# Kernel tuning notes

Measured on AMD Instinct MI355X. Metric: run time of the kernel, lower is better.

Reference implementation:

```python
import jax, jax.numpy as jnp
import numpy as np

B, T, D, H = 4, 1024, 1024, 16
DH = D // H  # 64

def setup_inputs() -> dict:
    key = jax.random.key(0)
    ks = jax.random.split(key, 5)
    s = 1.0 / np.sqrt(D)
    return {
        "x": jax.random.normal(ks[0], (B, T, D), dtype=jnp.float32),
        "Wqkv": jax.random.uniform(ks[1], (D, 3 * D), dtype=jnp.float32, minval=-s, maxval=s),
        "bqkv": jax.random.uniform(ks[2], (3 * D,), dtype=jnp.float32, minval=-s, maxval=s),
        "Wproj": jax.random.uniform(ks[3], (D, D), dtype=jnp.float32, minval=-s, maxval=s),
        "bproj": jax.random.uniform(ks[4], (D,), dtype=jnp.float32, minval=-s, maxval=s),
        "mask": jnp.ones((B, T), dtype=jnp.int32),
    }

def reference(x, Wqkv, bqkv, Wproj, bproj, mask):
    Bx, Tx, C = x.shape
    qkv = x @ Wqkv + bqkv                      # [B,T,3D]
    q, k, v = jnp.split(qkv, 3, axis=-1)
    # [B,H,T,DH]
    q = q.reshape(Bx, Tx, H, DH).transpose(0, 2, 1, 3)
    k = k.reshape(Bx, Tx, H, DH).transpose(0, 2, 1, 3)
    v = v.reshape(Bx, Tx, H, DH).transpose(0, 2, 1, 3)
    att = jnp.einsum("bhqd,bhkd->bhqk", q, k) / np.sqrt(DH)
    causal = jnp.tril(jnp.ones((Tx, Tx), dtype=bool))          # [T,T]
    keep = causal[None, None] & (mask[:, None, None, :] != 0)  # [B,1,T,T] broadcast
    att = jnp.where(keep, att, -jnp.inf)
    att = jax.nn.softmax(att, axis=-1)
    # dropout is identity in eval / p=0
    out = jnp.einsum("bhqk,bhkd->bhqd", att, v)                # [B,H,T,DH]
    out = out.transpose(0, 2, 1, 3).reshape(Bx, Tx, C)
    return out @ Wproj + bproj
```

## Files before the change

### kernel.cpp

```cpp
#include <hip/hip_runtime.h>
#include <hip/hip_bf16.h>
#include <cstddef>
#include <cstdint>

#define Bb 4
#define Tt 1024
#define Dd 1024
#define Hh 16

typedef __bf16 bf16x8 __attribute__((ext_vector_type(8)));
typedef __bf16 bf16x4 __attribute__((ext_vector_type(4)));
typedef float  f32x4  __attribute__((ext_vector_type(4)));

__device__ __forceinline__ void gload16(const void* g, void* l) {
    __builtin_amdgcn_global_load_lds(
        (const __attribute__((address_space(1))) void*)g,
        (__attribute__((address_space(3))) void*)l, 16, 0, 0);
}

__global__ __launch_bounds__(256) void prep(const float* __restrict__ x,
                                            const float* __restrict__ Wqkv,
                                            const float* __restrict__ Wproj,
                                            __bf16* __restrict__ xb,
                                            __bf16* __restrict__ wqT,
                                            __bf16* __restrict__ wpT) {
    const int bid = blockIdx.x;
    if (bid < 4096) {
        int i = bid * 256 + threadIdx.x;
        float4 v = ((const float4*)x)[i];
        bf16x4 o = { (__bf16)v.x, (__bf16)v.y, (__bf16)v.z, (__bf16)v.w };
        ((bf16x4*)xb)[i] = o;
        return;
    }
    __shared__ float ld[64][65];
    const float* in;
    __bf16* out;
    int K, N, k0, n0;
    if (bid < 4096 + 768) {
        int j = bid - 4096;
        in = Wqkv; out = wqT; K = 1024; N = 3072;
        k0 = (j & 15) * 64; n0 = (j >> 4) * 64;
    } else {
        int j = bid - 4096 - 768;
        in = Wproj; out = wpT; K = 1024; N = 1024;
        k0 = (j & 15) * 64; n0 = (j >> 4) * 64;
    }
    #pragma unroll
    for (int i = 0; i < 16; i++) {
        int idx = i * 256 + threadIdx.x;
        int r = idx >> 6, c = idx & 63;
        ld[r][c] = in[(size_t)(k0 + r) * N + n0 + c];
    }
    __syncthreads();
    #pragma unroll
    for (int i = 0; i < 16; i++) {
        int idx = i * 256 + threadIdx.x;
        int r = idx >> 6, c = idx & 63;
        out[(size_t)(n0 + r) * K + k0 + c] = (__bf16)ld[c][r];
    }
}

__global__ __launch_bounds__(256) void gemm_qkv(const __bf16* __restrict__ A,
                                                const __bf16* __restrict__ Bt,
                                                const float* __restrict__ bias,
                                                __bf16* __restrict__ Cout,
                                                __bf16* __restrict__ vt,
                                                int M, int N, int K) {
    __shared__ __align__(16) __bf16 smem[17408];
    __bf16* const As = smem;
    __bf16* const Bs = smem + 8192;

    const int tid  = threadIdx.x;
    const int lane = tid & 63;
    const int wave = tid >> 6;
    const int wy = wave >> 1, wx = wave & 1;
    const int l15 = lane & 15, quad = lane >> 4;
    const size_t row0 = (size_t)blockIdx.y * 128;
    const size_t col0 = (size_t)blockIdx.x * 128;

    f32x4 acc[4][4] = {};

    #pragma unroll
    for (int i = 0; i < 2; i++) {
        int c = i * 256 + tid;
        int r = c >> 2, seg = (c & 3) ^ ((r >> 1) & 3);
        gload16(&A[(row0 + r) * K + seg * 8], &As[c * 8]);
        gload16(&Bt[(col0 + r) * K + seg * 8], &Bs[c * 8]);
    }

    const int niter = K >> 5;
    for (int it = 0; it < niter; it++) {
        __syncthreads();
        const int cur = it & 1;
        if (it + 1 < niter) {
            const int k0 = (it + 1) << 5;
            #pragma unroll
            for (int i = 0; i < 2; i++) {
                int c = i * 256 + tid;
                int r = c >> 2, seg = (c & 3) ^ ((r >> 1) & 3);
                gload16(&A[(row0 + r) * K + k0 + seg * 8], &As[(cur ^ 1) * 4096 + c * 8]);
                gload16(&Bt[(col0 + r) * K + k0 + seg * 8], &Bs[(cur ^ 1) * 4096 + c * 8]);
            }
        }
        bf16x8 af[4], bfr[4];
        #pragma unroll
        for (int i = 0; i < 4; i++) {
            const int r = wy * 64 + i * 16 + l15;
            af[i] = *(const bf16x8*)&As[cur * 4096 + r * 32 + ((quad ^ ((r >> 1) & 3)) * 8)];
        }
        #pragma unroll
        for (int j = 0; j < 4; j++) {
            const int r = wx * 64 + j * 16 + l15;
            bfr[j] = *(const bf16x8*)&Bs[cur * 4096 + r * 32 + ((quad ^ ((r >> 1) & 3)) * 8)];
        }
        #pragma unroll
        for (int i = 0; i < 4; i++)
            #pragma unroll
            for (int j = 0; j < 4; j++)
                acc[i][j] = __builtin_amdgcn_mfma_f32_16x16x32_bf16(af[i], bfr[j], acc[i][j], 0, 0, 0);
    }

    __syncthreads();
    #pragma unroll
    for (int j = 0; j < 4; j++) {
        const int cl = wx * 64 + j * 16 + l15;
        const size_t col = col0 + cl;
        const float bj = bias[col];
        const float scale = (col < 1024) ? 0.125f : 1.0f;
        #pragma unroll
        for (int i = 0; i < 4; i++) {
            const int rl = wy * 64 + i * 16 + quad * 4;
            #pragma unroll
            for (int r = 0; r < 4; r++)
                smem[(rl + r) * 132 + cl] = (__bf16)((acc[i][j][r] + bj) * scale);
        }
    }
    __syncthreads();
    #pragma unroll
    for (int p = 0; p < 8; p++) {
        const int row = p * 16 + (tid >> 4);
        const int ch  = tid & 15;
        bf16x8 v = *(const bf16x8*)&smem[row * 132 + ch * 8];
        *(bf16x8*)&Cout[(row0 + row) * N + col0 + ch * 8] = v;
    }
    if (col0 >= 2048) {
        const int bidx = (int)(row0 >> 10);
        const int t0g  = (int)(row0 & 1023);
        const int cl   = tid >> 1;
        const int half = tid & 1;
        const int hd   = (int)(col0 - 2048) + cl;
        const size_t vrow = ((size_t)((bidx * Hh + (hd >> 6)) * 64 + (hd & 63))) * Tt + t0g;
        #pragma unroll
        for (int s = 0; s < 8; s++) {
            const int t = half * 64 + s * 8;
            bf16x8 v;
            #pragma unroll
            for (int u = 0; u < 8; u++) v[u] = smem[(t + u) * 132 + cl];
            *(bf16x8*)&vt[vrow + t] = v;
        }
    }
}

__global__ __launch_bounds__(256) void gemm_bf16_n64(const __bf16* __restrict__ A,
                                                     const __bf16* __restrict__ Bt,
                                                     const float* __restrict__ bias,
                                                     float* __restrict__ Cout,
                                                     int M, int N, int K) {
    __shared__ __align__(16) __bf16 As[128 * 64];
    __shared__ __align__(16) __bf16 Bs[64 * 64];
    const int tid  = threadIdx.x;
    const int lane = tid & 63;
    const int wave = tid >> 6;
    const int wy = wave >> 1, wx = wave & 1;
    const int l15 = lane & 15, quad = lane >> 4;
    const size_t row0 = (size_t)blockIdx.y * 128;
    const size_t col0 = (size_t)blockIdx.x * 64;

    f32x4 acc[4][2] = {};

    for (int k0 = 0; k0 < K; k0 += 64) {
        #pragma unroll
        for (int i = 0; i < 4; i++) {
            int c = i * 256 + tid;
            int r = c >> 3, seg = (c & 7) ^ (r & 7);
            gload16(&A[(row0 + r) * K + k0 + seg * 8], &As[c * 8]);
        }
        #pragma unroll
        for (int i = 0; i < 2; i++) {
            int c = i * 256 + tid;
            int r = c >> 3, seg = (c & 7) ^ (r & 7);
            gload16(&Bt[(col0 + r) * K + k0 + seg * 8], &Bs[c * 8]);
        }
        __syncthreads();
        #pragma unroll
        for (int kc = 0; kc < 2; kc++) {
            bf16x8 af[4], bfr[2];
            #pragma unroll
            for (int i = 0; i < 4; i++)
                af[i] = *(const bf16x8*)&As[(wy * 64 + i * 16 + l15) * 64 +
                                            (((kc * 4 + quad) ^ (l15 & 7)) * 8)];
            #pragma unroll
            for (int j = 0; j < 2; j++)
                bfr[j] = *(const bf16x8*)&Bs[(wx * 32 + j * 16 + l15) * 64 +
                                             (((kc * 4 + quad) ^ (l15 & 7)) * 8)];
            #pragma unroll
            for (int i = 0; i < 4; i++)
                #pragma unroll
                for (int j = 0; j < 2; j++)
                    acc[i][j] = __builtin_amdgcn_mfma_f32_16x16x32_bf16(af[i], bfr[j], acc[i][j], 0, 0, 0);
        }
        __syncthreads();
    }

    #pragma unroll
    for (int j = 0; j < 2; j++) {
        const size_t col = col0 + wx * 32 + j * 16 + l15;
        const float bj = bias[col];
        #pragma unroll
        for (int i = 0; i < 4; i++) {
            const size_t row = row0 + wy * 64 + i * 16 + quad * 4;
            #pragma unroll
            for (int r = 0; r < 4; r++)
                Cout[(row + r) * N + col] = acc[i][j][r] + bj;
        }
    }
}

__global__ __launch_bounds__(256, 4) void attn_mfma(const __bf16* __restrict__ qkv,
                                                    const __bf16* __restrict__ vt,
                                                    const int* __restrict__ mask,
                                                    __bf16* __restrict__ att) {
    __shared__ __align__(16) __bf16 Ks[2][4096];
    __shared__ __align__(16) __bf16 Vs[2][4096];
    __shared__ __align__(16) __bf16 Ps[4][1024];

    const int h  = blockIdx.x & 15;
    const int b  = blockIdx.x >> 4;
    const int qt = 15 - blockIdx.y;
    const int tid = threadIdx.x, lane = tid & 63, wave = tid >> 6;
    const int l15 = lane & 15, quad = lane >> 4;

    #pragma unroll
    for (int i = 0; i < 2; i++) {
        int c = i * 256 + tid;
        int rr = c >> 3, ch = c & 7;
        gload16(&qkv[((size_t)(b * Tt + qt * 64 + rr)) * 3072 + h * 64 + ((ch ^ (rr & 7)) * 8)],
                &Ks[0][c * 8]);
    }

    uint32_t mlo = 0, mhi = 0;
    for (int p = 0; p < 16; p++) {
        unsigned long long bal = __ballot(mask[b * Tt + p * 64 + lane] != 0);
        if ((lane & 15) == p) { mlo = (uint32_t)bal; mhi = (uint32_t)(bal >> 32); }
    }

    __syncthreads();
    bf16x8 qf0 = *(const bf16x8*)&Ks[0][(wave * 16 + l15) * 64 + ((quad ^ (l15 & 7)) * 8)];
    bf16x8 qf1 = *(const bf16x8*)&Ks[0][(wave * 16 + l15) * 64 + (((4 + quad) ^ (l15 & 7)) * 8)];
    __syncthreads();

    #pragma unroll
    for (int i = 0; i < 2; i++) {
        int c = i * 256 + tid;
        int rr = c >> 3, ch = c & 7, sw = ((ch ^ (rr & 7)) * 8);
        gload16(&qkv[((size_t)(b * Tt + rr)) * 3072 + 1024 + h * 64 + sw], &Ks[0][c * 8]);
        gload16(&vt[((size_t)((b * Hh + h) * 64 + rr)) * Tt + sw], &Vs[0][c * 8]);
    }

    f32x4 Oacc[4] = {};
    float lsum = 0.0f;

    for (int kt = 0; kt <= qt; kt++) {
        __syncthreads();
        const int cur = kt & 1;
        if (kt < qt) {
            #pragma unroll
            for (int i = 0; i < 2; i++) {
                int c = i * 256 + tid;
                int rr = c >> 3, ch = c & 7, sw = ((ch ^ (rr & 7)) * 8);
                gload16(&qkv[((size_t)(b * Tt + (kt + 1) * 64 + rr)) * 3072 + 1024 + h * 64 + sw],
                        &Ks[cur ^ 1][c * 8]);
                gload16(&vt[((size_t)((b * Hh + h) * 64 + rr)) * Tt + (kt + 1) * 64 + sw],
                        &Vs[cur ^ 1][c * 8]);
            }
        }

        const uint32_t lo = (uint32_t)__builtin_amdgcn_readlane((int)mlo, kt);
        const uint32_t hi = (uint32_t)__builtin_amdgcn_readlane((int)mhi, kt);

        bf16x8 ak[4][2];
        #pragma unroll
        for (int j = 0; j < 4; j++)
            #pragma unroll
            for (int kc = 0; kc < 2; kc++)
                ak[j][kc] = *(const bf16x8*)&Ks[cur][(j * 16 + l15) * 64 +
                                                     (((kc * 4 + quad) ^ (l15 & 7)) * 8)];
        #pragma unroll
        for (int j = 0; j < 4; j++) {
            f32x4 st = {};
            st = __builtin_amdgcn_mfma_f32_16x16x32_bf16(ak[j][0], qf0, st, 0, 0, 0);
            st = __builtin_amdgcn_mfma_f32_16x16x32_bf16(ak[j][1], qf1, st, 0, 0, 0);
            const uint32_t fld = (j < 2) ? (lo >> (j * 16)) : (hi >> ((j - 2) * 16));
            bf16x4 pv;
            #pragma unroll
            for (int r = 0; r < 4; r++) {
                const int tloc = j * 16 + quad * 4 + r;
                bool keep = (fld >> (quad * 4 + r)) & 1;
                if (kt == qt) keep = keep && (tloc <= wave * 16 + l15);
                const float pe = keep ? __expf(st[r]) : 0.0f;
                lsum += pe;
                pv[r] = (__bf16)pe;
            }
            *(bf16x4*)&Ps[wave][l15 * 64 + (((j * 4 + quad) ^ ((l15 & 7) << 1)) * 4)] = pv;
        }

        bf16x8 av[4][2];
        #pragma unroll
        for (int n = 0; n < 4; n++)
            #pragma unroll
            for (int kc = 0; kc < 2; kc++)
                av[n][kc] = *(const bf16x8*)&Vs[cur][(n * 16 + l15) * 64 +
                                                     (((kc * 4 + quad) ^ (l15 & 7)) * 8)];
        bf16x8 p0 = *(const bf16x8*)&Ps[wave][l15 * 64 + (((2 * quad) ^ ((l15 & 7) << 1)) * 4)];
        bf16x8 p1 = *(const bf16x8*)&Ps[wave][l15 * 64 + (((2 * (4 + quad)) ^ ((l15 & 7) << 1)) * 4)];
        #pragma unroll
        for (int n = 0; n < 4; n++) {
            Oacc[n] = __builtin_amdgcn_mfma_f32_16x16x32_bf16(av[n][0], p0, Oacc[n], 0, 0, 0);
            Oacc[n] = __builtin_amdgcn_mfma_f32_16x16x32_bf16(av[n][1], p1, Oacc[n], 0, 0, 0);
        }
    }

    float lt = lsum;
    lt += __shfl_xor(lt, 16);
    lt += __shfl_xor(lt, 32);
    const float inv = 1.0f / lt;
    const int q = qt * 64 + wave * 16 + l15;
    #pragma unroll
    for (int n = 0; n < 4; n++) {
        bf16x4 o;
        #pragma unroll
        for (int r = 0; r < 4; r++) o[r] = (__bf16)(Oacc[n][r] * inv);
        *(bf16x4*)&att[((size_t)(b * Tt + q)) * Dd + h * 64 + n * 16 + quad * 4] = o;
    }
}

extern "C" void kernel_launch(void* const* d_in, const int* in_sizes, int n_in,
                              void* d_out, int out_size, void* d_ws, size_t ws_size,
                              hipStream_t stream) {
    const float* x     = (const float*)d_in[0];
    const float* Wqkv  = (const float*)d_in[1];
    const float* bqkv  = (const float*)d_in[2];
    const float* Wproj = (const float*)d_in[3];
    const float* bproj = (const float*)d_in[4];
    const int*   mask  = (const int*)d_in[5];
    float* out = (float*)d_out;

    __bf16* xb  = (__bf16*)d_ws;
    __bf16* wqT = xb  + (size_t)4096 * 1024;
    __bf16* wpT = wqT + (size_t)3072 * 1024;
    __bf16* qkv = wpT + (size_t)1024 * 1024;
    __bf16* vt  = qkv + (size_t)4096 * 3072;
    __bf16* att = vt  + (size_t)4 * 16 * 64 * 1024;

    prep<<<4096 + 768 + 256, 256, 0, stream>>>(x, Wqkv, Wproj, xb, wqT, wpT);

    gemm_qkv<<<dim3(24, 32), 256, 0, stream>>>(xb, wqT, bqkv, qkv, vt, 4096, 3072, 1024);

    attn_mfma<<<dim3(64, 16), 256, 0, stream>>>(qkv, vt, mask, att);

    gemm_bf16_n64<<<dim3(16, 32), 256, 0, stream>>>(att, wpT, bproj, out, 4096, 1024, 1024);
}
```

Measured before the change: 163.2 us.

## Rewrite QKV GEMM as 256x256 tile with 8 waves and staged half-tile pipeline

Replaces the 128x128 QKV GEMM with a 256x256 tile, 512 threads and a K-step of 64. Global-to-LDS loads are split into half-tile stages that are interleaved between four MFMA quadrants, using explicit vmcnt/lgkmcnt waits, barriers and s_setprio. The aim is better data reuse and overlap of memory with compute. The cost is 128KB of LDS, a grid of only 192 blocks, and hand-tuned wait counts that are fragile.

```diff
diff --git a/kernel.cpp b/kernel.cpp
--- a/kernel.cpp
+++ b/kernel.cpp
@@ -60,104 +60,169 @@
     }
 }
 
-__global__ __launch_bounds__(256) void gemm_qkv(const __bf16* __restrict__ A,
-                                                const __bf16* __restrict__ Bt,
-                                                const float* __restrict__ bias,
-                                                __bf16* __restrict__ Cout,
-                                                __bf16* __restrict__ vt,
-                                                int M, int N, int K) {
-    __shared__ __align__(16) __bf16 smem[17408];
-    __bf16* const As = smem;
-    __bf16* const Bs = smem + 8192;
+__device__ __forceinline__ void stage_half(const __bf16* __restrict__ g,
+                                           __bf16* l, int tid) {
+    #pragma unroll
+    for (int s = 0; s < 2; ++s) {
+        const int c = s * 512 + tid;
+        const int r = c >> 3;
+        const int seg = (c & 7) ^ (r & 7);
+        gload16(&g[(size_t)r * 1024 + seg * 8], &l[c * 8]);
+    }
+}
+
+template <int MH>
+__device__ __forceinline__ void load_af(bf16x8 (&af)[4][2], const __bf16* AsC,
+                                        int wy, int l15, int quad) {
+    #pragma unroll
+    for (int mi = 0; mi < 4; ++mi)
+        #pragma unroll
+        for (int kc = 0; kc < 2; ++kc)
+            af[mi][kc] = *(const bf16x8*)&AsC[(wy * 128 + MH * 64 + mi * 16 + l15) * 64 +
+                                              (((kc * 4 + quad) ^ (l15 & 7)) * 8)];
+}
+
+template <int MH, int NH>
+__device__ __forceinline__ void mfma_quad(f32x4 (&acc)[8][4], const bf16x8 (&af)[4][2],
+                                          const bf16x8 (&bf)[4][2]) {
+    #pragma unroll
+    for (int mi = 0; mi < 4; ++mi)
+        #pragma unroll
+        for (int nj = 0; nj < 2; ++nj) {
+            f32x4 c = acc[MH * 4 + mi][NH * 2 + nj];
+            c = __builtin_amdgcn_mfma_f32_16x16x32_bf16(af[mi][0], bf[NH * 2 + nj][0], c, 0, 0, 0);
+            c = __builtin_amdgcn_mfma_f32_16x16x32_bf16(af[mi][1], bf[NH * 2 + nj][1], c, 0, 0, 0);
+            acc[MH * 4 + mi][NH * 2 + nj] = c;
+        }
+}
+
+__global__ __launch_bounds__(512, 2) void gemm_qkv(const __bf16* __restrict__ A,
+                                                   const __bf16* __restrict__ Bt,
+                                                   const float* __restrict__ bias,
+                                                   __bf16* __restrict__ Cout,
+                                                   __bf16* __restrict__ vt) {
+    constexpr int N = 3072;
+    constexpr int NT = 16;
+    __shared__ __align__(16) __bf16 smem[65536];
 
     const int tid  = threadIdx.x;
     const int lane = tid & 63;
     const int wave = tid >> 6;
-    const int wy = wave >> 1, wx = wave & 1;
+    const int wy = wave >> 2, wx = wave & 3;
     const int l15 = lane & 15, quad = lane >> 4;
-    const size_t row0 = (size_t)blockIdx.y * 128;
-    const size_t col0 = (size_t)blockIdx.x * 128;
-
-    f32x4 acc[4][4] = {};
-
-    #pragma unroll
-    for (int i = 0; i < 2; i++) {
-        int c = i * 256 + tid;
-        int r = c >> 2, seg = (c & 3) ^ ((r >> 1) & 3);
-        gload16(&A[(row0 + r) * K + seg * 8], &As[c * 8]);
-        gload16(&Bt[(col0 + r) * K + seg * 8], &Bs[c * 8]);
-    }
-
-    const int niter = K >> 5;
-    for (int it = 0; it < niter; it++) {
+    const size_t row0 = (size_t)blockIdx.y * 256;
+    const size_t col0 = (size_t)blockIdx.x * 256;
+
+    const __bf16* const Ab  = A  + row0 * 1024;
+    const __bf16* const Bb_ = Bt + col0 * 1024;
+
+    f32x4 acc[8][4] = {};
+    bf16x8 af[4][2], bf[4][2];
+
+    stage_half(Ab, smem, tid);
+    stage_half(Ab + (size_t)128 * 1024, smem + 8192, tid);
+    stage_half(Bb_, smem + 32768, tid);
+    stage_half(Bb_ + (size_t)128 * 1024, smem + 32768 + 8192, tid);
+    stage_half(Bb_ + 64, smem + 32768 + 16384, tid);
+    stage_half(Bb_ + (size_t)128 * 1024 + 64, smem + 32768 + 16384 + 8192, tid);
+    stage_half(Ab + 64, smem + 16384, tid);
+    asm volatile("s_waitcnt vmcnt(6)" ::: "memory");
+    __builtin_amdgcn_s_barrier();
+
+    for (int t = 0; t < NT; ++t) {
+        const int cur = t & 1;
+        __bf16* const AsC = smem + cur * 16384;
+        __bf16* const BsC = smem + 32768 + cur * 16384;
+        __bf16* const AsN = smem + (cur ^ 1) * 16384;
+
+        load_af<0>(af, AsC, wy, l15, quad);
+        #pragma unroll
+        for (int nj = 0; nj < 4; ++nj)
+            #pragma unroll
+            for (int kc = 0; kc < 2; ++kc)
+                bf[nj][kc] = *(const bf16x8*)&BsC[(wx * 64 + nj * 16 + l15) * 64 +
+                                                  (((kc * 4 + quad) ^ (l15 & 7)) * 8)];
+        if (t + 1 < NT) stage_half(Ab + (size_t)128 * 1024 + (t + 1) * 64, AsN + 8192, tid);
+        __builtin_amdgcn_s_barrier();
+        asm volatile("s_waitcnt lgkmcnt(0)" ::: "memory");
+        __builtin_amdgcn_s_setprio(1);
+        mfma_quad<0, 0>(acc, af, bf);
+        __builtin_amdgcn_s_setprio(0);
+        __builtin_amdgcn_s_barrier();
+
+        if (t + 2 < NT) stage_half(Bb_ + (t + 2) * 64, BsC, tid);
+        __builtin_amdgcn_s_barrier();
+        asm volatile("s_waitcnt lgkmcnt(0)" ::: "memory");
+        __builtin_amdgcn_s_setprio(1);
+        mfma_quad<0, 1>(acc, af, bf);
+        __builtin_amdgcn_s_setprio(0);
+        __builtin_amdgcn_s_barrier();
+
+        load_af<1>(af, AsC, wy, l15, quad);
+        if (t + 2 < NT) stage_half(Bb_ + (size_t)128 * 1024 + (t + 2) * 64, BsC + 8192, tid);
+        __builtin_amdgcn_s_barrier();
+        asm volatile("s_waitcnt lgkmcnt(0)" ::: "memory");
+        __builtin_amdgcn_s_setprio(1);
+        mfma_quad<1, 0>(acc, af, bf);
+        __builtin_amdgcn_s_setprio(0);
+        __builtin_amdgcn_s_barrier();
+
+        if (t + 2 < NT) stage_half(Ab + (t + 2) * 64, AsC, tid);
+        if (t + 2 < NT) {
+            asm volatile("s_waitcnt vmcnt(6)" ::: "memory");
+        } else if (t + 1 < NT) {
+            asm volatile("s_waitcnt vmcnt(0)" ::: "memory");
+        }
+        __builtin_amdgcn_s_barrier();
+        asm volatile("s_waitcnt lgkmcnt(0)" ::: "memory");
+        __builtin_amdgcn_s_setprio(1);
+        mfma_quad<1, 1>(acc, af, bf);
+        __builtin_amdgcn_s_setprio(0);
+        __builtin_amdgcn_s_barrier();
+    }
+
+    const float scale = (col0 < 1024) ? 0.125f : 1.0f;
+    const int isV = (col0 >= 2048);
+    for (int sl = 0; sl < 2; ++sl) {
+        if (wy == sl) {
+            #pragma unroll
+            for (int nj = 0; nj < 4; ++nj) {
+                const int cl = wx * 64 + nj * 16 + l15;
+                const float bj = bias[col0 + cl];
+                #pragma unroll
+                for (int mi = 0; mi < 8; ++mi) {
+                    #pragma unroll
+                    for (int r = 0; r < 4; ++r)
+                        smem[(mi * 16 + quad * 4 + r) * 264 + cl] =
+                            (__bf16)((acc[mi][nj][r] + bj) * scale);
+                }
+            }
+        }
         __syncthreads();
-        const int cur = it & 1;
-        if (it + 1 < niter) {
-            const int k0 = (it + 1) << 5;
-            #pragma unroll
-            for (int i = 0; i < 2; i++) {
-                int c = i * 256 + tid;
-                int r = c >> 2, seg = (c & 3) ^ ((r >> 1) & 3);
-                gload16(&A[(row0 + r) * K + k0 + seg * 8], &As[(cur ^ 1) * 4096 + c * 8]);
-                gload16(&Bt[(col0 + r) * K + k0 + seg * 8], &Bs[(cur ^ 1) * 4096 + c * 8]);
+        #pragma unroll
+        for (int p = 0; p < 8; ++p) {
+            const int idx = p * 512 + tid;
+            const int row = idx >> 5, ch = idx & 31;
+            bf16x8 v = *(const bf16x8*)&smem[row * 264 + ch * 8];
+            *(bf16x8*)&Cout[(row0 + sl * 128 + row) * N + col0 + ch * 8] = v;
+        }
+        if (isV) {
+            const int bidx = (int)(row0 >> 10);
+            const int t0g  = (int)(row0 & 1023) + sl * 128;
+            const int cl   = tid & 255;
+            const int th   = tid >> 8;
+            const int hd   = (int)(col0 - 2048) + cl;
+            const size_t vrow = ((size_t)((bidx * Hh + (hd >> 6)) * 64 + (hd & 63))) * Tt + t0g;
+            #pragma unroll
+            for (int p = 0; p < 8; ++p) {
+                const int tch = th * 8 + p;
+                bf16x8 v;
+                #pragma unroll
+                for (int u = 0; u < 8; ++u) v[u] = smem[(tch * 8 + u) * 264 + cl];
+                *(bf16x8*)&vt[vrow + tch * 8] = v;
             }
         }
-        bf16x8 af[4], bfr[4];
-        #pragma unroll
-        for (int i = 0; i < 4; i++) {
-            const int r = wy * 64 + i * 16 + l15;
-            af[i] = *(const bf16x8*)&As[cur * 4096 + r * 32 + ((quad ^ ((r >> 1) & 3)) * 8)];
-        }
-        #pragma unroll
-        for (int j = 0; j < 4; j++) {
-            const int r = wx * 64 + j * 16 + l15;
-            bfr[j] = *(const bf16x8*)&Bs[cur * 4096 + r * 32 + ((quad ^ ((r >> 1) & 3)) * 8)];
-        }
-        #pragma unroll
-        for (int i = 0; i < 4; i++)
-            #pragma unroll
-            for (int j = 0; j < 4; j++)
-                acc[i][j] = __builtin_amdgcn_mfma_f32_16x16x32_bf16(af[i], bfr[j], acc[i][j], 0, 0, 0);
-    }
-
-    __syncthreads();
-    #pragma unroll
-    for (int j = 0; j < 4; j++) {
-        const int cl = wx * 64 + j * 16 + l15;
-        const size_t col = col0 + cl;
-        const float bj = bias[col];
-        const float scale = (col < 1024) ? 0.125f : 1.0f;
-        #pragma unroll
-        for (int i = 0; i < 4; i++) {
-            const int rl = wy * 64 + i * 16 + quad * 4;
-            #pragma unroll
-            for (int r = 0; r < 4; r++)
-                smem[(rl + r) * 132 + cl] = (__bf16)((acc[i][j][r] + bj) * scale);
-        }
-    }
-    __syncthreads();
-    #pragma unroll
-    for (int p = 0; p < 8; p++) {
-        const int row = p * 16 + (tid >> 4);
-        const int ch  = tid & 15;
-        bf16x8 v = *(const bf16x8*)&smem[row * 132 + ch * 8];
-        *(bf16x8*)&Cout[(row0 + row) * N + col0 + ch * 8] = v;
-    }
-    if (col0 >= 2048) {
-        const int bidx = (int)(row0 >> 10);
-        const int t0g  = (int)(row0 & 1023);
-        const int cl   = tid >> 1;
-        const int half = tid & 1;
-        const int hd   = (int)(col0 - 2048) + cl;
-        const size_t vrow = ((size_t)((bidx * Hh + (hd >> 6)) * 64 + (hd & 63))) * Tt + t0g;
-        #pragma unroll
-        for (int s = 0; s < 8; s++) {
-            const int t = half * 64 + s * 8;
-            bf16x8 v;
-            #pragma unroll
-            for (int u = 0; u < 8; u++) v[u] = smem[(t + u) * 132 + cl];
-            *(bf16x8*)&vt[vrow + t] = v;
-        }
+        __syncthreads();
     }
 }
 
@@ -364,7 +429,7 @@
 
     prep<<<4096 + 768 + 256, 256, 0, stream>>>(x, Wqkv, Wproj, xb, wqT, wpT);
 
-    gemm_qkv<<<dim3(24, 32), 256, 0, stream>>>(xb, wqT, bqkv, qkv, vt, 4096, 3072, 1024);
+    gemm_qkv<<<dim3(12, 16), 512, 0, stream>>>(xb, wqT, bqkv, qkv, vt);
 
     attn_mfma<<<dim3(64, 16), 256, 0, stream>>>(qkv, vt, mask, att);
 
```

Measured after the change: 166.8 us. 2.2% more time.
